# Kernel tuning notes

Measured on AMD Instinct MI355X. Metric: run time of the kernel, lower is better.

The kernel has to match this reference:

```python
import jax, jax.numpy as jnp
import numpy as np

B, H, W, C, M1, M2, NL = 16, 41, 40, 48, 12, 12, 4
EPS = 1e-5
TX = jnp.linspace(0.0, 2.0 * np.pi, H, dtype=jnp.float32)      # theta grid, len 41
TY = jnp.linspace(0.0, 15.0, W, dtype=jnp.float32)             # z grid, len 40
DTX = 2.0 * np.pi / (H - 1)
DTY = 15.0 / (W - 1)
LAM1 = (2j * np.pi) * jnp.fft.fftfreq(H, d=DTX).astype(jnp.float32)  # [H] complex64
LAM2 = (2j * np.pi) * jnp.fft.fftfreq(W, d=DTY).astype(jnp.float32)  # [W] complex64


def setup_inputs() -> dict:
    key = jax.random.key(0)
    k = jax.random.split(key, 10)
    scale = 1.0 / (C * C)
    u = lambda kk, s: scale * jax.random.uniform(kk, s, dtype=jnp.float32)
    n = lambda kk, s, sc: sc * jax.random.normal(kk, s, dtype=jnp.float32)
    return {
        "x": n(k[0], (B, H, W, 1), 1.0),
        "fc0_w": n(k[1], (C, 3), 0.3), "fc0_b": jnp.zeros((C,), jnp.float32),
        "poles1": u(k[2], (NL, C, C, M1, 2)),          # real/imag split of cfloat params
        "poles2": u(k[3], (NL, C, C, M2, 2)),
        "residues": u(k[4], (NL, C, C, M1, M2, 2)),
        "conv_w": n(k[5], (NL, C, C), 1.0 / np.sqrt(C)), "conv_b": jnp.zeros((NL, C), jnp.float32),
        "fc1_w": n(k[6], (128, C), 1.0 / np.sqrt(C)), "fc1_b": jnp.zeros((128,), jnp.float32),
        "fc2_w": n(k[7], (2, 128), 1.0 / np.sqrt(128)), "fc2_b": jnp.zeros((2,), jnp.float32),
    }


def _cplx(a):
    return a[..., 0] + 1j * a[..., 1]


def _inorm(h):  # InstanceNorm2d(affine=False): per-(b,c) over H,W, biased var
    m = h.mean(axis=(-2, -1), keepdims=True)
    v = h.var(axis=(-2, -1), keepdims=True)
    return (h - m) / jnp.sqrt(v + EPS)


def _pr2d(h, p1ri, p2ri, resri):
    # h: [B,C,H,W] real. Pole-residue Laplace spectral operator (PR2d.forward).
    p1 = _cplx(p1ri)     # [Ci,Co,M1]
    p2 = _cplx(p2ri)     # [Ci,Co,M2]
    res = _cplx(resri)   # [Ci,Co,M1,M2]
    alpha = jnp.fft.fft2(h, axes=(-2, -1))                      # [B,Ci,H,W] complex
    inv1 = 1.0 / (LAM1[None, None, None, :] - p1[..., None])    # [Ci,Co,M1,H]
    inv2 = 1.0 / (LAM2[None, None, None, :] - p2[..., None])    # [Ci,Co,M2,W]
    # output_residue1[b,k,o,x] = sum_{i,p,q} alpha * res * inv1 * inv2
    S = jnp.einsum('ikpq,ikpo,ikqx->ikox', res, inv1, inv2)     # [Ci,Co,H,W]
    res1 = jnp.einsum('biox,ikox->bkox', alpha, S)              # [B,Co,H,W]
    # output_residue2[b,k,p,q] = sum_{i,o,x} alpha * res * inv1 * inv2
    A = jnp.einsum('biox,ikpo->bikpx', alpha, inv1)             # [B,Ci,Co,M1,W]
    G = jnp.einsum('bikpx,ikqx->bikpq', A, inv2)                # [B,Ci,Co,M1,M2]
    r2 = jnp.einsum('bikpq,ikpq->bkpq', G, res)                 # [B,Co,M1,M2]
    x1 = jnp.fft.ifft2(res1, axes=(-2, -1)).real
    # reconstruction: exp(pole * t) outer products (term1/term2/term3 in torch)
    E1 = jnp.exp(p1[..., None] * TX[None, None, None, :])       # [Ci,Co,M1,H]
    E2 = jnp.exp(p2[..., None] * TY[None, None, None, :])       # [Ci,Co,M2,W]
    U = jnp.einsum('kbpq,bipz->kbiqz', r2, E1)                  # [B,Ci,Co,M2,H]
    x2 = jnp.einsum('kbiqz,biqx->kizx', U, E2).real / (H * W)   # [B,Co,H,W]
    return x1 + x2


def reference(x, fc0_w, fc0_b, poles1, poles2, residues, conv_w, conv_b,
              fc1_w, fc1_b, fc2_w, fc2_b):
    b = x.shape[0]
    gx = jnp.broadcast_to(jnp.linspace(0.0, 1.0, H, dtype=jnp.float32)[None, :, None, None], (b, H, W, 1))
    gy = jnp.broadcast_to(jnp.linspace(0.0, 1.0, W, dtype=jnp.float32)[None, None, :, None], (b, H, W, 1))
    h = jnp.concatenate([x, gx, gy], axis=-1)                   # [B,H,W,3]
    h = jnp.einsum('bhwi,ci->bhwc', h, fc0_w) + fc0_b           # fc0
    h = jnp.transpose(h, (0, 3, 1, 2))                          # [B,C,H,W]
    for l in range(NL):
        x1 = _inorm(_pr2d(_inorm(h), poles1[l], poles2[l], residues[l]))
        x2 = jnp.einsum('oi,bihw->bohw', conv_w[l], h) + conv_b[l][None, :, None, None]
        h = jnp.sin(x1 + x2)
    h = jnp.transpose(h, (0, 2, 3, 1))                          # [B,H,W,C]
    h = jnp.sin(jnp.einsum('bhwc,oc->bhwo', h, fc1_w) + fc1_b)
    out = jnp.einsum('bhwc,oc->bhwo', h, fc2_w) + fc2_b         # [B,H,W,2]
    return out
```

## Files before the change

kernel.cpp:

```cpp
#include <hip/hip_runtime.h>
#include <math.h>

#define DI __device__ __forceinline__

constexpr int B = 16, H = 41, W = 40, C = 48, M1 = 12, M2 = 12, NL = 4;
constexpr int HW = H * W;
constexpr float EPS = 1e-5f;
constexpr float PI_F = 3.14159265358979323846f;

__device__ float  g_h[2][B * C * HW];
__device__ float2 g_alpha[B * C * HW];
__device__ float2 g_inv1t[NL][C * C][H * 16];
__device__ float2 g_inv2a[NL][C * C][M2 * W];
__device__ float2 g_E1a[NL][C * C][M1 * H];
__device__ float2 g_E2a[NL][C * C][M2 * W];
__device__ float2 g_Sa[NL][C * C][HW];
__device__ float2 g_res1[B * C * HW];
__device__ float  g_x1[B * C * HW];
__device__ float2 g_r2[B * C * M1 * M2];
__device__ float2 g_Zr[C * C][B * M1 * M2];
__device__ float  g_xpart[3][B * C][HW];
__device__ float  g_mu[B * C];
__device__ float  g_rstd[B * C];
__device__ float2 g_wfh[H * H];
__device__ float2 g_wfw[W * W];

DI float2 cmadd(float2 a, float2 b, float2 acc) {
    acc.x = fmaf(a.x, b.x, fmaf(-a.y, b.y, acc.x));
    acc.y = fmaf(a.x, b.y, fmaf(a.y, b.x, acc.y));
    return acc;
}
DI float2 cmul(float2 a, float2 b) {
    return make_float2(a.x * b.x - a.y * b.y, a.x * b.y + a.y * b.x);
}

__global__ void k_tw() {
    int tid = blockIdx.x * 256 + threadIdx.x;
    if (tid < H * H) {
        int o = tid / H, h = tid % H;
        float ph = -2.0f * PI_F * (float)((o * h) % H) / (float)H;
        float s, c; sincosf(ph, &s, &c);
        g_wfh[tid] = make_float2(c, s);
    }
    int t2 = tid - H * H;
    if (t2 >= 0 && t2 < W * W) {
        int o = t2 / W, w = t2 % W;
        float ph = -2.0f * PI_F * (float)((o * w) % W) / (float)W;
        float s, c; sincosf(ph, &s, &c);
        g_wfw[t2] = make_float2(c, s);
    }
}

__global__ void k_fc0(const float* __restrict__ x, const float* __restrict__ w,
                      const float* __restrict__ bias) {
    int idx = blockIdx.x * 256 + threadIdx.x;
    if (idx >= B * C * HW) return;
    int hw = idx % HW; int bc = idx / HW; int c = bc % C; int b = bc / C;
    int hh = hw / W, ww = hw % W;
    float xv = x[b * HW + hw];
    float gx = hh * (1.0f / (H - 1));
    float gy = ww * (1.0f / (W - 1));
    g_h[0][idx] = fmaf(w[c * 3 + 0], xv, fmaf(w[c * 3 + 1], gx, fmaf(w[c * 3 + 2], gy, bias[c])));
}

__global__ __launch_bounds__(256) void k_fft(int src) {
    int bid = blockIdx.x;
    const float* hp = &g_h[src][(size_t)bid * HW];
    __shared__ float sh[HW];
    __shared__ float2 st[HW];
    __shared__ float2 swf[H * H];
    __shared__ float red[8];
    int tid = threadIdx.x;
    float s = 0.f, ss = 0.f;
    for (int i = tid; i < HW; i += 256) { float v = hp[i]; sh[i] = v; s += v; ss += v * v; }
    for (int i = tid; i < H * H; i += 256) swf[i] = g_wfh[i];
    for (int off = 32; off; off >>= 1) { s += __shfl_down(s, off); ss += __shfl_down(ss, off); }
    if ((tid & 63) == 0) { red[tid >> 6] = s; red[4 + (tid >> 6)] = ss; }
    __syncthreads();
    if (tid == 0) {
        float S = red[0] + red[1] + red[2] + red[3];
        float SS = red[4] + red[5] + red[6] + red[7];
        float mean = S * (1.0f / HW);
        float var = SS * (1.0f / HW) - mean * mean;
        red[0] = mean; red[1] = rsqrtf(var + EPS);
    }
    __syncthreads();
    float mean = red[0], rstd = red[1];
    for (int i = tid; i < HW; i += 256) sh[i] = (sh[i] - mean) * rstd;
    __syncthreads();
    for (int i = tid; i < 21 * W; i += 256) {
        int o0 = (i / W) * 2, w = i % W;
        bool pair = (o0 + 1) < H;
        float2 a0 = make_float2(0.f, 0.f), a1 = make_float2(0.f, 0.f);
        for (int h = 0; h < H; h++) {
            float v = sh[h * W + w];
            float2 t0 = swf[o0 * H + h];
            a0.x = fmaf(t0.x, v, a0.x); a0.y = fmaf(t0.y, v, a0.y);
            if (pair) {
                float2 t1 = swf[o0 * H + H + h];
                a1.x = fmaf(t1.x, v, a1.x); a1.y = fmaf(t1.y, v, a1.y);
            }
        }
        st[o0 * W + w] = a0;
        if (pair) st[(o0 + 1) * W + w] = a1;
    }
    __syncthreads();
    for (int t = tid; t < W * W; t += 256) {
        int x = t / W, w = t % W;
        swf[x * 41 + w] = g_wfw[t];
    }
    __syncthreads();
    float2* ap = &g_alpha[(size_t)bid * HW];
    for (int i = tid; i < H * 20; i += 256) {
        int o = i / 20, x0 = (i % 20) * 2;
        float2 a0 = make_float2(0.f, 0.f), a1 = make_float2(0.f, 0.f);
        for (int w = 0; w < W; w++) {
            float2 sv = st[o * W + w];
            a0 = cmadd(sv, swf[x0 * 41 + w], a0);
            a1 = cmadd(sv, swf[(x0 + 1) * 41 + w], a1);
        }
        ap[o * W + x0] = a0;
        ap[o * W + x0 + 1] = a1;
    }
}

__global__ __launch_bounds__(256) void k_tbS(const float* __restrict__ p1, const float* __restrict__ p2,
                                             const float* __restrict__ res_in) {
    int gb = blockIdx.x;
    int l = gb / (C * C), pk = gb % (C * C);
    int tid = threadIdx.x;
    __shared__ float2 sinv1[M1 * H];
    __shared__ float2 sinv2[M2 * W];
    __shared__ float2 sT[M1 * W];
    __shared__ float2 sres[M1 * M2];
    const float* pp1 = p1 + (size_t)gb * M1 * 2;
    const float* pp2 = p2 + (size_t)gb * M2 * 2;
    for (int t = tid; t < M1 * H; t += 256) {
        int p = t / H, o = t % H;
        float pr = pp1[p * 2], pi = pp1[p * 2 + 1];
        int ko = (o <= H / 2) ? o : o - H;
        float lam = (40.0f / 41.0f) * (float)ko;
        float a = -pr, b = lam - pi;
        float d = 1.0f / (a * a + b * b);
        float2 inv = make_float2(a * d, -b * d);
        sinv1[t] = inv;
        float tt = o * (2.0f * PI_F / (H - 1));
        float er = expf(pr * tt);
        float sn, cs; sincosf(pi * tt, &sn, &cs);
        g_E1a[l][pk][t] = make_float2(er * cs, er * sn);
    }
    for (int t = tid; t < M2 * W; t += 256) {
        int q = t / W, x = t % W;
        float pr = pp2[q * 2], pi = pp2[q * 2 + 1];
        int kx = (x < W / 2) ? x : x - W;
        float lam = (2.0f * PI_F * 39.0f / 600.0f) * (float)kx;
        float a = -pr, b = lam - pi;
        float d = 1.0f / (a * a + b * b);
        float2 inv = make_float2(a * d, -b * d);
        sinv2[t] = inv;
        g_inv2a[l][pk][t] = inv;
        float tt = x * (15.0f / (W - 1));
        float er = expf(pr * tt);
        float sn, cs; sincosf(pi * tt, &sn, &cs);
        g_E2a[l][pk][t] = make_float2(er * cs, er * sn);
    }
    const float2* rp = (const float2*)res_in + (size_t)gb * M1 * M2;
    for (int t = tid; t < M1 * M2; t += 256) sres[t] = rp[t];
    __syncthreads();
    for (int t = tid; t < H * 16; t += 256) {
        int o = t >> 4, p = t & 15;
        g_inv1t[l][pk][t] = (p < M1) ? sinv1[p * H + o] : make_float2(0.f, 0.f);
    }
    for (int t = tid; t < M1 * W; t += 256) {
        int p = t / W, x = t % W;
        float2 acc = make_float2(0.f, 0.f);
        for (int q = 0; q < M2; q++) acc = cmadd(sres[p * M2 + q], sinv2[q * W + x], acc);
        sT[t] = acc;
    }
    __syncthreads();
    float2* sp = g_Sa[l][pk];
    for (int t = tid; t < HW; t += 256) {
        int o = t / W, x = t % W;
        float2 acc = make_float2(0.f, 0.f);
        for (int p = 0; p < M1; p++) acc = cmadd(sinv1[p * H + o], sT[p * W + x], acc);
        sp[t] = acc;
    }
}

__global__ __launch_bounds__(256) void k_res1(int l) {
    int bid = blockIdx.x;
    int ch = bid % 7;
    int rest = bid / 7;
    int kq = rest % 12, bp = rest / 12;
    int hw = ch * 256 + threadIdx.x;
    if (hw >= HW) return;
    int b0 = bp * 2, k0 = kq * 4;
    float2 acc[2][4];
#pragma unroll
    for (int u = 0; u < 2; u++)
#pragma unroll
        for (int v = 0; v < 4; v++) acc[u][v] = make_float2(0.f, 0.f);
    for (int i = 0; i < C; i++) {
        float2 a0 = g_alpha[(size_t)((b0    ) * C + i) * HW + hw];
        float2 a1 = g_alpha[(size_t)((b0 + 1) * C + i) * HW + hw];
        float2 s0 = g_Sa[l][i * C + k0][hw];
        float2 s1 = g_Sa[l][i * C + k0 + 1][hw];
        float2 s2 = g_Sa[l][i * C + k0 + 2][hw];
        float2 s3 = g_Sa[l][i * C + k0 + 3][hw];
        acc[0][0] = cmadd(a0, s0, acc[0][0]);
        acc[0][1] = cmadd(a0, s1, acc[0][1]);
        acc[0][2] = cmadd(a0, s2, acc[0][2]);
        acc[0][3] = cmadd(a0, s3, acc[0][3]);
        acc[1][0] = cmadd(a1, s0, acc[1][0]);
        acc[1][1] = cmadd(a1, s1, acc[1][1]);
        acc[1][2] = cmadd(a1, s2, acc[1][2]);
        acc[1][3] = cmadd(a1, s3, acc[1][3]);
    }
#pragma unroll
    for (int u = 0; u < 2; u++)
#pragma unroll
        for (int v = 0; v < 4; v++)
            g_res1[(size_t)((b0 + u) * C + k0 + v) * HW + hw] = acc[u][v];
}

__global__ __launch_bounds__(256) void k_ifft() {
    int bid = blockIdx.x; int tid = threadIdx.x;
    __shared__ float2 s0[HW], s1[HW];
    __shared__ float2 swf[H * H];
    const float2* rp = &g_res1[(size_t)bid * HW];
    for (int i = tid; i < HW; i += 256) s0[i] = rp[i];
    for (int i = tid; i < H * H; i += 256) swf[i] = g_wfh[i];
    __syncthreads();
    for (int i = tid; i < 21 * W; i += 256) {
        int h0 = (i / W) * 2, x = i % W;
        bool pair = (h0 + 1) < H;
        float2 a0 = make_float2(0.f, 0.f), a1 = make_float2(0.f, 0.f);
        for (int o = 0; o < H; o++) {
            float2 v = s0[o * W + x];
            float2 t0 = swf[o * H + h0];
            a0.x = fmaf(v.x, t0.x, fmaf(v.y, t0.y, a0.x));
            a0.y = fmaf(v.y, t0.x, fmaf(-v.x, t0.y, a0.y));
            if (pair) {
                float2 t1 = swf[o * H + h0 + 1];
                a1.x = fmaf(v.x, t1.x, fmaf(v.y, t1.y, a1.x));
                a1.y = fmaf(v.y, t1.x, fmaf(-v.x, t1.y, a1.y));
            }
        }
        s1[h0 * W + x] = a0;
        if (pair) s1[(h0 + 1) * W + x] = a1;
    }
    __syncthreads();
    for (int t = tid; t < W * W; t += 256) {
        int x = t / W, w = t % W;
        swf[x * 41 + w] = g_wfw[t];
    }
    __syncthreads();
    float* xp = &g_x1[(size_t)bid * HW];
    for (int i = tid; i < H * 20; i += 256) {
        int h = i / 20, w0 = (i % 20) * 2;
        float a0 = 0.f, a1 = 0.f;
        for (int x = 0; x < W; x++) {
            float2 v = s1[h * W + x];
            float2 t0 = swf[x * 41 + w0];
            float2 t1 = swf[x * 41 + w0 + 1];
            a0 = fmaf(v.x, t0.x, fmaf(v.y, t0.y, a0));
            a1 = fmaf(v.x, t1.x, fmaf(v.y, t1.y, a1));
        }
        xp[h * W + w0]     = a0 * (1.0f / (H * W));
        xp[h * W + w0 + 1] = a1 * (1.0f / (H * W));
    }
}

__global__ __launch_bounds__(256) void k_r2a(const float* __restrict__ res_in, int l) {
    int bid = blockIdx.x;
    int xcd = bid & 7, idx = bid >> 3;
    int i = (idx / (C * 4)) * 8 + xcd;
    int rem = idx % (C * 4);
    int k = rem >> 2;
    int bc = rem & 3;
    int pk = i * C + k;
    int tid = threadIdx.x;
    __shared__ float2 sY[4 * M1 * 41];
    __shared__ float2 si1t[H * 16];
    __shared__ float2 si2[M2 * 41];
    __shared__ float2 sres[M1 * M2];
    for (int t = tid; t < H * 16; t += 256) si1t[t] = g_inv1t[l][pk][t];
    for (int t = tid; t < M2 * W; t += 256) {
        int q = t / W, x = t % W;
        si2[q * 41 + x] = g_inv2a[l][pk][t];
    }
    const float2* rp = (const float2*)res_in + (size_t)(l * C * C + pk) * M1 * M2;
    for (int t = tid; t < M1 * M2; t += 256) sres[t] = rp[t];
    __syncthreads();
    if (tid < 160) {
        int bloc = tid / 40, x = tid % 40;
        int b = bc * 4 + bloc;
        const float2* ap = &g_alpha[(size_t)(b * C + i) * HW + x];
        float2 yacc[12];
#pragma unroll
        for (int p = 0; p < 12; p++) yacc[p] = make_float2(0.f, 0.f);
        for (int o = 0; o < H; o++) {
            float2 a = ap[o * W];
            const float4* e4 = (const float4*)&si1t[o * 16];
#pragma unroll
            for (int j = 0; j < 6; j++) {
                float4 ee = e4[j];
                yacc[2 * j]     = cmadd(make_float2(ee.x, ee.y), a, yacc[2 * j]);
                yacc[2 * j + 1] = cmadd(make_float2(ee.z, ee.w), a, yacc[2 * j + 1]);
            }
        }
#pragma unroll
        for (int p = 0; p < 12; p++) sY[(bloc * M1 + p) * 41 + x] = yacc[p];
    }
    __syncthreads();
    if (tid < 192) {
        int bloc = tid / 48, rem2 = tid % 48;
        int p = rem2 >> 2, qq = rem2 & 3;
        int q0 = qq * 3;
        float2 zacc[3];
#pragma unroll
        for (int j = 0; j < 3; j++) zacc[j] = make_float2(0.f, 0.f);
        const float2* yrow = &sY[(bloc * M1 + p) * 41];
        for (int x = 0; x < W; x++) {
            float2 y = yrow[x];
#pragma unroll
            for (int j = 0; j < 3; j++) zacc[j] = cmadd(y, si2[(q0 + j) * 41 + x], zacc[j]);
        }
        int b = bc * 4 + bloc;
        float2* out = &g_Zr[pk][b * (M1 * M2) + p * M2 + q0];
#pragma unroll
        for (int j = 0; j < 3; j++) out[j] = cmul(sres[p * M2 + q0 + j], zacc[j]);
    }
}

__global__ __launch_bounds__(256) void k_r2b() {
    int t = blockIdx.x * 256 + threadIdx.x;
    if (t >= B * C * M1 * M2) return;
    int pq = t % (M1 * M2);
    int k = (t / (M1 * M2)) % C;
    int b = t / (M1 * M2 * C);
    float2 acc = make_float2(0.f, 0.f);
    for (int i = 0; i < C; i++) {
        float2 v = g_Zr[i * C + k][b * (M1 * M2) + pq];
        acc.x += v.x; acc.y += v.y;
    }
    g_r2[(size_t)(b * C + k) * (M1 * M2) + pq] = acc;
}

constexpr int XNCI = 2;
__global__ __launch_bounds__(256) void k_x2p(int l) {
    int bid = blockIdx.x;
    int xcd = bid & 7, rest = bid >> 3;
    int part = rest % 3;
    int idx = rest / 3;
    int k = (idx / B) * 8 + xcd;
    int b = idx % B;
    int tid = threadIdx.x;
    __shared__ float2 sE1[XNCI * M1 * 44];
    __shared__ float2 sV [XNCI * M1 * 40];
    __shared__ float2 sE2[XNCI * M2 * 41];
    __shared__ float2 sr2[XNCI * M1 * M2];
    int xh = tid % 20, zq = tid / 20;
    int x0 = xh * 2, z0 = zq * 4;
    float accr[4][2];
#pragma unroll
    for (int zi = 0; zi < 4; zi++) { accr[zi][0] = 0.f; accr[zi][1] = 0.f; }

    int cg0 = part * (C / XNCI / 3);
    for (int cg = cg0; cg < cg0 + C / XNCI / 3; cg++) {
        for (int t = tid; t < XNCI * M1 * 44; t += 256) {
            int j = t / (M1 * 44), rem = t % (M1 * 44);
            int p = rem / 44, z = rem % 44;
            sE1[t] = (z < H) ? g_E1a[l][(cg * XNCI + j) * C + k][p * H + z]
                             : make_float2(0.f, 0.f);
        }
        for (int t = tid; t < XNCI * M2 * W; t += 256) {
            int j = t / (M2 * W), rem = t % (M2 * W);
            sE2[(t / W) * 41 + (t % W)] = g_E2a[l][(cg * XNCI + j) * C + k][rem];
        }
        for (int t = tid; t < XNCI * M1 * M2; t += 256) {
            int j = t / (M1 * M2);
            sr2[t] = g_r2[(size_t)(b * C + cg * XNCI + j) * (M1 * M2) + (t % (M1 * M2))];
        }
        __syncthreads();
        for (int r = 0; r < 2; r++) {
            int id = tid + r * 256;
            if (id < XNCI * 6 * W) {
                int j = id / (6 * W), rem = id % (6 * W);
                int pp = rem / W, x = rem % W;
                int p0 = pp * 2;
                float2 a0 = make_float2(0.f, 0.f), a1 = make_float2(0.f, 0.f);
#pragma unroll
                for (int q = 0; q < M2; q++) {
                    float2 e = sE2[(j * M2 + q) * 41 + x];
                    a0 = cmadd(sr2[j * (M1 * M2) + p0 * M2 + q], e, a0);
                    a1 = cmadd(sr2[j * (M1 * M2) + (p0 + 1) * M2 + q], e, a1);
                }
                sV[(j * M1 + p0) * 40 + x] = a0;
                sV[(j * M1 + p0 + 1) * 40 + x] = a1;
            }
        }
        __syncthreads();
        if (tid < 240 && z0 < H) {
            for (int jp = 0; jp < XNCI * M1; jp++) {
                float4 v  = *(const float4*)&sV[jp * 40 + x0];
                float4 eA = *(const float4*)&sE1[jp * 44 + z0];
                float4 eB = *(const float4*)&sE1[jp * 44 + z0 + 2];
                accr[0][0] = fmaf(eA.x, v.x, fmaf(-eA.y, v.y, accr[0][0]));
                accr[0][1] = fmaf(eA.x, v.z, fmaf(-eA.y, v.w, accr[0][1]));
                accr[1][0] = fmaf(eA.z, v.x, fmaf(-eA.w, v.y, accr[1][0]));
                accr[1][1] = fmaf(eA.z, v.z, fmaf(-eA.w, v.w, accr[1][1]));
                accr[2][0] = fmaf(eB.x, v.x, fmaf(-eB.y, v.y, accr[2][0]));
                accr[2][1] = fmaf(eB.x, v.z, fmaf(-eB.y, v.w, accr[2][1]));
                accr[3][0] = fmaf(eB.z, v.x, fmaf(-eB.w, v.y, accr[3][0]));
                accr[3][1] = fmaf(eB.z, v.z, fmaf(-eB.w, v.w, accr[3][1]));
            }
        }
        __syncthreads();
    }
    float* op = &g_xpart[part][b * C + k][0];
    if (tid < 240 && z0 < H) {
#pragma unroll
        for (int zi = 0; zi < 4; zi++) {
            int z = z0 + zi;
            if (z < H) { op[z * W + x0] = accr[zi][0]; op[z * W + x0 + 1] = accr[zi][1]; }
        }
    }
}

__global__ __launch_bounds__(256) void k_fin() {
    int bid = blockIdx.x;
    int tid = threadIdx.x;
    __shared__ float red[8];
    float* xp = &g_x1[(size_t)bid * HW];
    const float* p0 = &g_xpart[0][bid][0];
    const float* p1 = &g_xpart[1][bid][0];
    const float* p2 = &g_xpart[2][bid][0];
    float s = 0.f, ss = 0.f;
    for (int i = tid; i < HW; i += 256) {
        float v = xp[i] + (p0[i] + p1[i] + p2[i]) * (1.0f / (H * W));
        xp[i] = v; s += v; ss += v * v;
    }
    for (int off = 32; off; off >>= 1) { s += __shfl_down(s, off); ss += __shfl_down(ss, off); }
    if ((tid & 63) == 0) { red[tid >> 6] = s; red[4 + (tid >> 6)] = ss; }
    __syncthreads();
    if (tid == 0) {
        float S = red[0] + red[1] + red[2] + red[3];
        float SS = red[4] + red[5] + red[6] + red[7];
        float mean = S * (1.0f / HW);
        float var = SS * (1.0f / HW) - mean * mean;
        g_mu[bid] = mean; g_rstd[bid] = rsqrtf(var + EPS);
    }
}

constexpr int TILE = 128;
constexpr int NTILE = (HW + TILE - 1) / TILE;
__global__ __launch_bounds__(256) void k_comb(const float* __restrict__ cw,
                                              const float* __restrict__ cb, int l, int src) {
    int b = blockIdx.x / NTILE;
    int t0 = (blockIdx.x % NTILE) * TILE;
    int tid = threadIdx.x;
    __shared__ float shh[C * TILE];
    __shared__ float scw[C * C];
    __shared__ float smu[C], srs[C], scb[C];
    for (int i = tid; i < C * C; i += 256) scw[i] = cw[l * C * C + i];
    for (int i = tid; i < C; i += 256) {
        smu[i] = g_mu[b * C + i]; srs[i] = g_rstd[b * C + i]; scb[i] = cb[l * C + i];
    }
    for (int i = tid; i < C * TILE; i += 256) {
        int c = i / TILE, t = i % TILE; int hw = t0 + t;
        shh[i] = (hw < HW) ? g_h[src][(size_t)(b * C + c) * HW + hw] : 0.f;
    }
    __syncthreads();
    for (int i = tid; i < C * TILE; i += 256) {
        int o = i / TILE, t = i % TILE; int hw = t0 + t;
        if (hw >= HW) continue;
        float acc = scb[o];
        for (int ci = 0; ci < C; ci++) acc = fmaf(scw[o * C + ci], shh[ci * TILE + t], acc);
        float prn = (g_x1[(size_t)(b * C + o) * HW + hw] - smu[o]) * srs[o];
        g_h[src ^ 1][(size_t)(b * C + o) * HW + hw] = sinf(prn + acc);
    }
}

__global__ __launch_bounds__(256) void k_head(const float* __restrict__ w1, const float* __restrict__ b1,
                                              const float* __restrict__ w2, const float* __restrict__ b2,
                                              float* __restrict__ out, int src) {
    __shared__ float sw1[128 * C];
    __shared__ float sb1[128], sw2[2 * 128];
    int tid = threadIdx.x;
    for (int i = tid; i < 128 * C; i += 256) sw1[i] = w1[i];
    for (int i = tid; i < 128; i += 256) sb1[i] = b1[i];
    for (int i = tid; i < 256; i += 256) sw2[i] = w2[i];
    __syncthreads();
    int pt = blockIdx.x * 256 + tid;
    if (pt >= B * HW) return;
    int b = pt / HW, hw = pt % HW;
    float hv[C];
#pragma unroll
    for (int c = 0; c < C; c++) hv[c] = g_h[src][(size_t)(b * C + c) * HW + hw];
    float o0 = b2[0], o1 = b2[1];
    for (int j = 0; j < 128; j++) {
        float a = sb1[j];
#pragma unroll
        for (int c = 0; c < C; c++) a = fmaf(sw1[j * C + c], hv[c], a);
        float sv = sinf(a);
        o0 = fmaf(sw2[j], sv, o0);
        o1 = fmaf(sw2[128 + j], sv, o1);
    }
    out[pt * 2 + 0] = o0; out[pt * 2 + 1] = o1;
}

extern "C" void kernel_launch(void* const* d_in, const int* in_sizes, int n_in,
                              void* d_out, int out_size, void* d_ws, size_t ws_size,
                              hipStream_t stream) {
    const float* x    = (const float*)d_in[0];
    const float* fc0w = (const float*)d_in[1];
    const float* fc0b = (const float*)d_in[2];
    const float* p1   = (const float*)d_in[3];
    const float* p2   = (const float*)d_in[4];
    const float* res  = (const float*)d_in[5];
    const float* cw   = (const float*)d_in[6];
    const float* cb   = (const float*)d_in[7];
    const float* w1   = (const float*)d_in[8];
    const float* b1   = (const float*)d_in[9];
    const float* w2   = (const float*)d_in[10];
    const float* b2   = (const float*)d_in[11];
    float* out = (float*)d_out;

    k_tw<<<(H * H + W * W + 255) / 256, 256, 0, stream>>>();
    k_fc0<<<(B * C * HW + 255) / 256, 256, 0, stream>>>(x, fc0w, fc0b);
    k_tbS<<<NL * C * C, 256, 0, stream>>>(p1, p2, res);
    int src = 0;
    for (int l = 0; l < NL; l++) {
        k_fft<<<B * C, 256, 0, stream>>>(src);
        k_res1<<<672, 256, 0, stream>>>(l);
        k_ifft<<<B * C, 256, 0, stream>>>();
        k_r2a<<<C * C * 4, 256, 0, stream>>>(res, l);
        k_r2b<<<(B * C * M1 * M2 + 255) / 256, 256, 0, stream>>>();
        k_x2p<<<3 * B * C, 256, 0, stream>>>(l);
        k_fin<<<B * C, 256, 0, stream>>>();
        k_comb<<<B * NTILE, 256, 0, stream>>>(cw, cb, l, src);
        src ^= 1;
    }
    k_head<<<(B * HW + 255) / 256, 256, 0, stream>>>(w1, b1, w2, b2, out, src);
}
```

Baseline: 1.901 ms.

## Fuse inverse FFT with instance-norm finalize and widen r2a thread mapping

The inverse 2D DFT kernel now runs after the x2 partial kernel and also adds the three x2 partials, writes x1, and computes the per-(b,c) mean and rstd. This removes the separate finalize kernel and one read/write pass over x1. Separately, k_r2a moves to 320 threads: two groups of 160 threads each compute half of the M1 modes in the first stage, and 288 threads compute two q outputs each in the second stage. The aim is more parallelism and fewer registers per thread, at the cost of more blocks' worth of threads competing for occupancy.

```diff
diff --git a/kernel.cpp b/kernel.cpp
--- a/kernel.cpp
+++ b/kernel.cpp
@@ -223,10 +223,11 @@
             g_res1[(size_t)((b0 + u) * C + k0 + v) * HW + hw] = acc[u][v];
 }
 
-__global__ __launch_bounds__(256) void k_ifft() {
+__global__ __launch_bounds__(256) void k_ifftfin() {
     int bid = blockIdx.x; int tid = threadIdx.x;
     __shared__ float2 s0[HW], s1[HW];
     __shared__ float2 swf[H * H];
+    __shared__ float red[8];
     const float2* rp = &g_res1[(size_t)bid * HW];
     for (int i = tid; i < HW; i += 256) s0[i] = rp[i];
     for (int i = tid; i < H * H; i += 256) swf[i] = g_wfh[i];
@@ -256,6 +257,10 @@
     }
     __syncthreads();
     float* xp = &g_x1[(size_t)bid * HW];
+    const float* q0p = &g_xpart[0][bid][0];
+    const float* q1p = &g_xpart[1][bid][0];
+    const float* q2p = &g_xpart[2][bid][0];
+    float s = 0.f, ss = 0.f;
     for (int i = tid; i < H * 20; i += 256) {
         int h = i / 20, w0 = (i % 20) * 2;
         float a0 = 0.f, a1 = 0.f;
@@ -266,12 +271,25 @@
             a0 = fmaf(v.x, t0.x, fmaf(v.y, t0.y, a0));
             a1 = fmaf(v.x, t1.x, fmaf(v.y, t1.y, a1));
         }
-        xp[h * W + w0]     = a0 * (1.0f / (H * W));
-        xp[h * W + w0 + 1] = a1 * (1.0f / (H * W));
-    }
-}
-
-__global__ __launch_bounds__(256) void k_r2a(const float* __restrict__ res_in, int l) {
+        int id0 = h * W + w0;
+        float v0 = (a0 + q0p[id0] + q1p[id0] + q2p[id0]) * (1.0f / (H * W));
+        float v1 = (a1 + q0p[id0 + 1] + q1p[id0 + 1] + q2p[id0 + 1]) * (1.0f / (H * W));
+        xp[id0] = v0; xp[id0 + 1] = v1;
+        s += v0 + v1; ss += v0 * v0 + v1 * v1;
+    }
+    for (int off = 32; off; off >>= 1) { s += __shfl_down(s, off); ss += __shfl_down(ss, off); }
+    if ((tid & 63) == 0) { red[tid >> 6] = s; red[4 + (tid >> 6)] = ss; }
+    __syncthreads();
+    if (tid == 0) {
+        float S = red[0] + red[1] + red[2] + red[3];
+        float SS = red[4] + red[5] + red[6] + red[7];
+        float mean = S * (1.0f / HW);
+        float var = SS * (1.0f / HW) - mean * mean;
+        g_mu[bid] = mean; g_rstd[bid] = rsqrtf(var + EPS);
+    }
+}
+
+__global__ __launch_bounds__(320) void k_r2a(const float* __restrict__ res_in, int l) {
     int bid = blockIdx.x;
     int xcd = bid & 7, idx = bid >> 3;
     int i = (idx / (C * 4)) * 8 + xcd;
@@ -284,52 +302,55 @@
     __shared__ float2 si1t[H * 16];
     __shared__ float2 si2[M2 * 41];
     __shared__ float2 sres[M1 * M2];
-    for (int t = tid; t < H * 16; t += 256) si1t[t] = g_inv1t[l][pk][t];
-    for (int t = tid; t < M2 * W; t += 256) {
+    for (int t = tid; t < H * 16; t += 320) si1t[t] = g_inv1t[l][pk][t];
+    for (int t = tid; t < M2 * W; t += 320) {
         int q = t / W, x = t % W;
         si2[q * 41 + x] = g_inv2a[l][pk][t];
     }
     const float2* rp = (const float2*)res_in + (size_t)(l * C * C + pk) * M1 * M2;
-    for (int t = tid; t < M1 * M2; t += 256) sres[t] = rp[t];
-    __syncthreads();
-    if (tid < 160) {
-        int bloc = tid / 40, x = tid % 40;
+    for (int t = tid; t < M1 * M2; t += 320) sres[t] = rp[t];
+    __syncthreads();
+    {
+        int ph = tid / 160;
+        int r2t = tid % 160;
+        int bloc = r2t / 40, x = r2t % 40;
         int b = bc * 4 + bloc;
+        int p0 = ph * 6;
         const float2* ap = &g_alpha[(size_t)(b * C + i) * HW + x];
-        float2 yacc[12];
-#pragma unroll
-        for (int p = 0; p < 12; p++) yacc[p] = make_float2(0.f, 0.f);
+        float2 yacc[6];
+#pragma unroll
+        for (int p = 0; p < 6; p++) yacc[p] = make_float2(0.f, 0.f);
         for (int o = 0; o < H; o++) {
             float2 a = ap[o * W];
-            const float4* e4 = (const float4*)&si1t[o * 16];
-#pragma unroll
-            for (int j = 0; j < 6; j++) {
+            const float4* e4 = (const float4*)&si1t[o * 16 + p0];
+#pragma unroll
+            for (int j = 0; j < 3; j++) {
                 float4 ee = e4[j];
                 yacc[2 * j]     = cmadd(make_float2(ee.x, ee.y), a, yacc[2 * j]);
                 yacc[2 * j + 1] = cmadd(make_float2(ee.z, ee.w), a, yacc[2 * j + 1]);
             }
         }
 #pragma unroll
-        for (int p = 0; p < 12; p++) sY[(bloc * M1 + p) * 41 + x] = yacc[p];
-    }
-    __syncthreads();
-    if (tid < 192) {
-        int bloc = tid / 48, rem2 = tid % 48;
-        int p = rem2 >> 2, qq = rem2 & 3;
-        int q0 = qq * 3;
-        float2 zacc[3];
-#pragma unroll
-        for (int j = 0; j < 3; j++) zacc[j] = make_float2(0.f, 0.f);
+        for (int p = 0; p < 6; p++) sY[(bloc * M1 + p0 + p) * 41 + x] = yacc[p];
+    }
+    __syncthreads();
+    if (tid < 288) {
+        int bloc = tid / 72, rem2 = tid % 72;
+        int p = rem2 / 6, qh = rem2 % 6;
+        int q0 = qh * 2;
+        float2 zacc0 = make_float2(0.f, 0.f), zacc1 = make_float2(0.f, 0.f);
         const float2* yrow = &sY[(bloc * M1 + p) * 41];
+        const float2* s2a = &si2[q0 * 41];
+        const float2* s2b = &si2[(q0 + 1) * 41];
         for (int x = 0; x < W; x++) {
             float2 y = yrow[x];
-#pragma unroll
-            for (int j = 0; j < 3; j++) zacc[j] = cmadd(y, si2[(q0 + j) * 41 + x], zacc[j]);
+            zacc0 = cmadd(y, s2a[x], zacc0);
+            zacc1 = cmadd(y, s2b[x], zacc1);
         }
         int b = bc * 4 + bloc;
         float2* out = &g_Zr[pk][b * (M1 * M2) + p * M2 + q0];
-#pragma unroll
-        for (int j = 0; j < 3; j++) out[j] = cmul(sres[p * M2 + q0 + j], zacc[j]);
+        out[0] = cmul(sres[p * M2 + q0], zacc0);
+        out[1] = cmul(sres[p * M2 + q0 + 1], zacc1);
     }
 }
 
@@ -428,31 +449,6 @@
     }
 }
 
-__global__ __launch_bounds__(256) void k_fin() {
-    int bid = blockIdx.x;
-    int tid = threadIdx.x;
-    __shared__ float red[8];
-    float* xp = &g_x1[(size_t)bid * HW];
-    const float* p0 = &g_xpart[0][bid][0];
-    const float* p1 = &g_xpart[1][bid][0];
-    const float* p2 = &g_xpart[2][bid][0];
-    float s = 0.f, ss = 0.f;
-    for (int i = tid; i < HW; i += 256) {
-        float v = xp[i] + (p0[i] + p1[i] + p2[i]) * (1.0f / (H * W));
-        xp[i] = v; s += v; ss += v * v;
-    }
-    for (int off = 32; off; off >>= 1) { s += __shfl_down(s, off); ss += __shfl_down(ss, off); }
-    if ((tid & 63) == 0) { red[tid >> 6] = s; red[4 + (tid >> 6)] = ss; }
-    __syncthreads();
-    if (tid == 0) {
-        float S = red[0] + red[1] + red[2] + red[3];
-        float SS = red[4] + red[5] + red[6] + red[7];
-        float mean = S * (1.0f / HW);
-        float var = SS * (1.0f / HW) - mean * mean;
-        g_mu[bid] = mean; g_rstd[bid] = rsqrtf(var + EPS);
-    }
-}
-
 constexpr int TILE = 128;
 constexpr int NTILE = (HW + TILE - 1) / TILE;
 __global__ __launch_bounds__(256) void k_comb(const float* __restrict__ cw,
@@ -534,11 +530,10 @@
     for (int l = 0; l < NL; l++) {
         k_fft<<<B * C, 256, 0, stream>>>(src);
         k_res1<<<672, 256, 0, stream>>>(l);
-        k_ifft<<<B * C, 256, 0, stream>>>();
-        k_r2a<<<C * C * 4, 256, 0, stream>>>(res, l);
+        k_r2a<<<C * C * 4, 320, 0, stream>>>(res, l);
         k_r2b<<<(B * C * M1 * M2 + 255) / 256, 256, 0, stream>>>();
         k_x2p<<<3 * B * C, 256, 0, stream>>>(l);
-        k_fin<<<B * C, 256, 0, stream>>>();
+        k_ifftfin<<<B * C, 256, 0, stream>>>();
         k_comb<<<B * NTILE, 256, 0, stream>>>(cw, cb, l, src);
         src ^= 1;
     }
```

Result: faster. 1.779 ms (-6.4%).
